# Performance work log

Measured on AMD Instinct MI355X. Metric: run time of the kernel, lower is better.

Reference implementation:

```python
import jax, jax.numpy as jnp
import numpy as np

N, E, F = 20000, 160000, 128
H, C1, C2 = 4, 128, 256
G, NCLS = 64, 10


def setup_inputs() -> dict:
    key = jax.random.key(0)
    ks = jax.random.split(key, 14)
    s = 0.05
    inp = {
        "x": jax.random.normal(ks[0], (N, F), jnp.float32),
        "edge_index": jax.random.randint(ks[1], (2, E), 0, N, dtype=jnp.int32),
        "batch": ((jnp.arange(N, dtype=jnp.int32) * G) // N),  # sorted graph ids, all 64 graphs non-empty
        # GATConv 1: in=128 -> 128 per head, heads=4, concat -> 512
        "W1": jax.random.normal(ks[2], (F, H * C1), jnp.float32) * s,
        "att_src1": jax.random.normal(ks[3], (H, C1), jnp.float32) * s,
        "att_dst1": jax.random.normal(ks[4], (H, C1), jnp.float32) * s,
        "b1": jnp.zeros((H * C1,), jnp.float32),
        # GATConv 2: in=512 -> 256, heads=1, concat=False
        "W2": jax.random.normal(ks[5], (H * C1, C2), jnp.float32) * s,
        "att_src2": jax.random.normal(ks[6], (1, C2), jnp.float32) * s,
        "att_dst2": jax.random.normal(ks[7], (1, C2), jnp.float32) * s,
        "b2": jnp.zeros((C2,), jnp.float32),
        # fc head
        "fc1_w": jax.random.normal(ks[8], (C2, 64), jnp.float32) * s,
        "fc1_b": jnp.zeros((64,), jnp.float32),
        "fc2_w": jax.random.normal(ks[9], (64, NCLS), jnp.float32) * s,
        "fc2_b": jnp.zeros((NCLS,), jnp.float32),
    }
    return inp


def gat_conv(x, src, dst, W, att_src, att_dst, bias, concat):
    """PyG GATConv: per-edge attention + segment softmax over dst + scatter-add."""
    n = x.shape[0]
    h_, c_ = att_src.shape
    h = (x @ W).reshape(n, h_, c_)                    # [N,H,C]
    a_src = jnp.einsum('nhc,hc->nh', h, att_src)       # [N,H]
    a_dst = jnp.einsum('nhc,hc->nh', h, att_dst)       # [N,H]
    e = jax.nn.leaky_relu(a_src[src] + a_dst[dst], negative_slope=0.2)  # [Etot,H]
    e_max = jax.ops.segment_max(e, dst, num_segments=n)
    ee = jnp.exp(e - e_max[dst])
    denom = jax.ops.segment_sum(ee, dst, num_segments=n)
    alpha = ee / denom[dst]                            # [Etot,H]
    out = jax.ops.segment_sum(h[src] * alpha[:, :, None], dst, num_segments=n)  # [N,H,C]
    out = out.reshape(n, h_ * c_) if concat else out.mean(axis=1)
    return out + bias


def reference(x, edge_index, batch, W1, att_src1, att_dst1, b1,
              W2, att_src2, att_dst2, b2, fc1_w, fc1_b, fc2_w, fc2_b):
    n = x.shape[0]
    # to_undirected: both directions; plus self-loops (GATConv add_self_loops=True)
    loops = jnp.arange(n, dtype=edge_index.dtype)
    src = jnp.concatenate([edge_index[0], edge_index[1], loops])
    dst = jnp.concatenate([edge_index[1], edge_index[0], loops])
    h = gat_conv(x, src, dst, W1, att_src1, att_dst1, b1, concat=True)
    h = jax.nn.relu(h)
    h = gat_conv(h, src, dst, W2, att_src2, att_dst2, b2, concat=False)
    g = jax.ops.segment_max(h, batch, num_segments=G)  # global_max_pool
    g = jax.nn.relu(g @ fc1_w + fc1_b) @ fc2_w + fc2_b
    return jax.nn.log_softmax(g, axis=1)
```

## Files before the change

### kernel.cpp

```cpp
#include <hip/hip_runtime.h>
#include <math.h>

#define FDIM 128
#define HEADS 4
#define C1DIM 128
#define C2DIM 256
#define NGRAPH 64
#define NCLS 10
#define DEGCAP 64

typedef __attribute__((ext_vector_type(8))) short short8;
typedef __attribute__((ext_vector_type(4))) float float4v;
typedef __attribute__((ext_vector_type(2))) float floatx2;

__device__ __forceinline__ unsigned short f2bf(float f) {
    unsigned u = __builtin_bit_cast(unsigned, f);
    unsigned r = (u + 0x7FFFu + ((u >> 16) & 1u)) >> 16;
    return (unsigned short)r;
}
__device__ __forceinline__ float bfu(unsigned short u) { return __builtin_bit_cast(float, (unsigned)u << 16); }
__device__ __forceinline__ float lrelu(float x) { return x > 0.f ? x : 0.2f * x; }
__device__ __forceinline__ float sel4(float a, float b, float c, float d, int hd) {
    return hd == 0 ? a : hd == 1 ? b : hd == 2 ? c : d;
}
__device__ __forceinline__ unsigned char f2fp8(float f) {
    return (unsigned char)(__builtin_amdgcn_cvt_pk_fp8_f32(f, f, 0, false) & 0xff);
}
__device__ __forceinline__ void fp8x8_dec(int2 r, float* f) {
    floatx2 p0 = __builtin_amdgcn_cvt_pk_f32_fp8(r.x, false);
    floatx2 p1 = __builtin_amdgcn_cvt_pk_f32_fp8(r.x, true);
    floatx2 p2 = __builtin_amdgcn_cvt_pk_f32_fp8(r.y, false);
    floatx2 p3 = __builtin_amdgcn_cvt_pk_f32_fp8(r.y, true);
    f[0] = p0.x; f[1] = p0.y; f[2] = p1.x; f[3] = p1.y;
    f[4] = p2.x; f[5] = p2.y; f[6] = p3.x; f[7] = p3.y;
}
__device__ __forceinline__ void fp8x4_dec(int r, float* f) {
    floatx2 p0 = __builtin_amdgcn_cvt_pk_f32_fp8(r, false);
    floatx2 p1 = __builtin_amdgcn_cvt_pk_f32_fp8(r, true);
    f[0] = p0.x; f[1] = p0.y; f[2] = p1.x; f[3] = p1.y;
}
__device__ __forceinline__ unsigned encf(float v) {
    unsigned b = __builtin_bit_cast(unsigned, v);
    return (b & 0x80000000u) ? ~b : (b | 0x80000000u);
}
__device__ __forceinline__ float decf(unsigned u) {
    unsigned b = (u & 0x80000000u) ? (u ^ 0x80000000u) : ~u;
    return __builtin_bit_cast(float, b);
}

__global__ __launch_bounds__(256) void prep_kernel(
        int* __restrict__ zero_base, int nzero_words,
        const float* __restrict__ x, unsigned short* __restrict__ xb, int n4,
        const float* __restrict__ W1, unsigned short* __restrict__ W1t,
        const float* __restrict__ W2, unsigned short* __restrict__ W2t,
        int ZB, int CB) {
    __shared__ float tile[32][33];
    int blk = blockIdx.x;
    if (blk < ZB) {
        int i = blk * 256 + threadIdx.x;
        if (i < nzero_words) zero_base[i] = 0;
        return;
    }
    blk -= ZB;
    if (blk < CB) {
        int i = blk * 256 + threadIdx.x;
        if (i < n4) {
            float4 v = ((const float4*)x)[i];
            ushort4 o;
            o.x = f2bf(v.x); o.y = f2bf(v.y); o.z = f2bf(v.z); o.w = f2bf(v.w);
            ((ushort4*)xb)[i] = o;
        }
        return;
    }
    blk -= CB;
    const float* W; unsigned short* Wt; int K, Nc, bx, by;
    if (blk < 64) {
        W = W1; Wt = W1t; K = 128; Nc = 512;
        bx = (blk & 15) * 32; by = (blk >> 4) * 32;
    } else {
        blk -= 64;
        W = W2; Wt = W2t; K = 512; Nc = 256;
        bx = (blk & 7) * 32; by = (blk >> 3) * 32;
    }
    int tx = threadIdx.x & 31, ty = threadIdx.x >> 5;
    #pragma unroll
    for (int r = 0; r < 32; r += 8)
        tile[ty + r][tx] = W[(size_t)(by + ty + r) * Nc + bx + tx];
    __syncthreads();
    #pragma unroll
    for (int r = 0; r < 32; r += 8)
        Wt[(size_t)(bx + ty + r) * K + by + tx] = f2bf(tile[tx][ty + r]);
}

template<int MODE>
__global__ __launch_bounds__(256) void bgemm_kernel(
        const unsigned short* __restrict__ A,
        const unsigned short* __restrict__ Bt,
        unsigned char* __restrict__ Cout,
        const float* __restrict__ att_src,
        const float* __restrict__ att_dst,
        float* __restrict__ as_out,
        float* __restrict__ ad_out,
        int M, int N_, int K,
        const int* __restrict__ ei, int E,
        int* __restrict__ cnt, int* __restrict__ esrc, int SB) {
    if (MODE == 1 && blockIdx.x < SB) {
        int i = blockIdx.x * 256 + threadIdx.x;
        if (i < 2 * E) {
            int src = ei[i];
            int dst = (i < E) ? ei[E + i] : ei[i - E];
            int pos = atomicAdd(&cnt[dst], 1);
            if (pos < DEGCAP) esrc[(dst << 6) + pos] = src;
        }
        return;
    }
    constexpr int BN = (MODE == 1) ? 128 : 256;
    constexpr int JW = BN / 32;
    constexpr int CPADB = BN + 16;
    constexpr int SMEMB = 4096 + BN * 64;
    __shared__ __align__(16) unsigned char smem[SMEMB];
    unsigned short* As = (unsigned short*)smem;
    unsigned short* Bs = (unsigned short*)(smem + 4096);
    __shared__ float sd_s[4][32];
    __shared__ float sd_d[4][32];
    const int t = threadIdx.x;
    const int lane = t & 63;
    const int wave = t >> 6;
    int row0, col0, headi;
    if (MODE == 1) {
        int bb = blockIdx.x - SB;
        headi = bb & 3;
        col0 = headi * BN;
        row0 = (bb >> 2) * 64;
    } else {
        headi = 0;
        col0 = 0;
        row0 = blockIdx.x * 64;
    }
    const int wr = (wave >> 1) * 32, wc = (wave & 1) * (BN / 2);
    float4v acc[2][JW] = {};
    for (int k0 = 0; k0 < K; k0 += 32) {
        {
            int i = t;
            int gr = row0 + (i >> 2); if (gr >= M) gr = M - 1;
            const unsigned short* gp = A + (size_t)gr * K + k0 + ((i & 3) << 3);
            __builtin_amdgcn_global_load_lds(
                (const __attribute__((address_space(1))) unsigned int*)gp,
                (__attribute__((address_space(3))) unsigned int*)&As[i * 8], 16, 0, 0);
        }
        #pragma unroll
        for (int c = 0; c < BN / 64; ++c) {
            int i = c * 256 + t;
            int gn = col0 + (i >> 2);
            const unsigned short* gp = Bt + (size_t)gn * K + k0 + ((i & 3) << 3);
            __builtin_amdgcn_global_load_lds(
                (const __attribute__((address_space(1))) unsigned int*)gp,
                (__attribute__((address_space(3))) unsigned int*)&Bs[i * 8], 16, 0, 0);
        }
        __syncthreads();
        short8 af[2], bfr[JW];
        #pragma unroll
        for (int i = 0; i < 2; ++i)
            af[i] = *(const short8*)&As[(wr + i * 16 + (lane & 15)) * 32 + (lane >> 4) * 8];
        #pragma unroll
        for (int j = 0; j < JW; ++j)
            bfr[j] = *(const short8*)&Bs[(wc + j * 16 + (lane & 15)) * 32 + (lane >> 4) * 8];
        #pragma unroll
        for (int i = 0; i < 2; ++i)
            #pragma unroll
            for (int j = 0; j < JW; ++j)
                acc[i][j] = __builtin_amdgcn_mfma_f32_16x16x32_bf16(af[i], bfr[j], acc[i][j], 0, 0, 0);
        __syncthreads();
    }
    float asv[JW], adv[JW];
    #pragma unroll
    for (int j = 0; j < JW; ++j) {
        int cc = col0 + wc + j * 16 + (lane & 15);
        asv[j] = att_src[cc];
        adv[j] = att_dst[cc];
    }
    #pragma unroll
    for (int i = 0; i < 2; ++i) {
        #pragma unroll
        for (int p = 0; p < 4; ++p) {
            int rr = wr + i * 16 + (lane >> 4) * 4 + p;
            float s = 0.f, d = 0.f;
            #pragma unroll
            for (int j = 0; j < JW; ++j) {
                smem[rr * CPADB + wc + j * 16 + (lane & 15)] = f2fp8(acc[i][j][p]);
                s += acc[i][j][p] * asv[j];
                d += acc[i][j][p] * adv[j];
            }
            #pragma unroll
            for (int o = 1; o <= 8; o <<= 1) { s += __shfl_xor(s, o); d += __shfl_xor(d, o); }
            if ((lane & 15) == 0) {
                int ridx = i * 16 + (lane >> 4) * 4 + p;
                sd_s[wave][ridx] = s;
                sd_d[wave][ridx] = d;
            }
        }
    }
    __syncthreads();
    #pragma unroll
    for (int it = 0; it < BN / 64; ++it) {
        int idx = it * 256 + t;
        int row = idx / (BN / 16), c16 = (idx % (BN / 16)) * 16;
        int grw = row0 + row;
        if (grw < M)
            *(int4*)&Cout[(size_t)grw * N_ + col0 + c16] = *(const int4*)&smem[row * CPADB + c16];
    }
    if ((wave & 1) == 0 && lane < 32) {
        float s = sd_s[wave][lane] + sd_s[wave + 1][lane];
        float d = sd_d[wave][lane] + sd_d[wave + 1][lane];
        int r = row0 + wr + lane;
        if (r < M) {
            if (MODE == 1) {
                as_out[r * 4 + headi] = s;
                ad_out[r * 4 + headi] = d;
            } else {
                as_out[r] = s;
                ad_out[r] = d;
            }
        }
    }
}

__global__ __launch_bounds__(256) void edge_agg1_kernel(
        const unsigned char* __restrict__ h1f8,
        const float4* __restrict__ as14,
        const float4* __restrict__ ad14,
        const int* __restrict__ cnt,
        const int* __restrict__ esrc,
        const float* __restrict__ b1,
        unsigned short* __restrict__ ho1b, int N) {
    __shared__ int sl_s[4][64];
    __shared__ __align__(16) float4 w_s[4][64];
    int wave = threadIdx.x >> 6, lane = threadIdx.x & 63;
    int node = blockIdx.x * 4 + wave;
    if (node >= N) return;
    int deg = cnt[node]; if (deg > DEGCAP) deg = DEGCAP;
    int ebase = node << 6;
    float4 asn = as14[node], adn = ad14[node];
    float w0 = __expf(lrelu(asn.x + adn.x));
    float w1 = __expf(lrelu(asn.y + adn.y));
    float w2 = __expf(lrelu(asn.z + adn.z));
    float w3 = __expf(lrelu(asn.w + adn.w));
    int hd = lane >> 4;
    int c0 = lane * 8;
    float wsh = sel4(w0, w1, w2, w3, hd);
    float acc[8];
    {
        int2 rs = *(const int2*)&h1f8[(size_t)node * 512 + c0];
        float f[8]; fp8x8_dec(rs, f);
        #pragma unroll
        for (int k = 0; k < 8; ++k) acc[k] = wsh * f[k];
    }
    float d0 = 0.f, d1 = 0.f, d2 = 0.f, d3 = 0.f;
    for (int cb = 0; cb < deg; cb += 64) {
        int idx = cb + lane;
        int sl = esrc[ebase + (idx < deg ? idx : deg - 1)];
        float4 wl = make_float4(0.f, 0.f, 0.f, 0.f);
        if (idx < deg) {
            float4 a = as14[sl];
            wl.x = __expf(lrelu(a.x + adn.x));
            wl.y = __expf(lrelu(a.y + adn.y));
            wl.z = __expf(lrelu(a.z + adn.z));
            wl.w = __expf(lrelu(a.w + adn.w));
            d0 += wl.x; d1 += wl.y; d2 += wl.z; d3 += wl.w;
        }
        sl_s[wave][lane] = sl;
        w_s[wave][lane] = wl;
        int jmax = deg - cb; if (jmax > 64) jmax = 64;
        int j = 0;
        for (; j + 4 <= jmax; j += 4) {
            int s0 = sl_s[wave][j],     s1 = sl_s[wave][j + 1];
            int s2 = sl_s[wave][j + 2], s3 = sl_s[wave][j + 3];
            float u0 = ((const float*)&w_s[wave][j])[hd];
            float u1 = ((const float*)&w_s[wave][j + 1])[hd];
            float u2 = ((const float*)&w_s[wave][j + 2])[hd];
            float u3 = ((const float*)&w_s[wave][j + 3])[hd];
            int2 r0 = *(const int2*)&h1f8[(size_t)s0 * 512 + c0];
            int2 r1 = *(const int2*)&h1f8[(size_t)s1 * 512 + c0];
            int2 r2 = *(const int2*)&h1f8[(size_t)s2 * 512 + c0];
            int2 r3 = *(const int2*)&h1f8[(size_t)s3 * 512 + c0];
            float f0[8], f1[8], f2[8], f3[8];
            fp8x8_dec(r0, f0); fp8x8_dec(r1, f1); fp8x8_dec(r2, f2); fp8x8_dec(r3, f3);
            #pragma unroll
            for (int k = 0; k < 8; ++k)
                acc[k] += u0 * f0[k] + u1 * f1[k] + u2 * f2[k] + u3 * f3[k];
        }
        for (; j < jmax; ++j) {
            int s = sl_s[wave][j];
            float u = ((const float*)&w_s[wave][j])[hd];
            int2 r = *(const int2*)&h1f8[(size_t)s * 512 + c0];
            float f[8]; fp8x8_dec(r, f);
            #pragma unroll
            for (int k = 0; k < 8; ++k) acc[k] += u * f[k];
        }
    }
    #pragma unroll
    for (int o = 32; o > 0; o >>= 1) {
        d0 += __shfl_xor(d0, o); d1 += __shfl_xor(d1, o);
        d2 += __shfl_xor(d2, o); d3 += __shfl_xor(d3, o);
    }
    d0 += w0; d1 += w1; d2 += w2; d3 += w3;
    float dh = sel4(d0, d1, d2, d3, hd);
    float inv = 1.f / dh;
    float4 bA = *(const float4*)&b1[c0], bB = *(const float4*)&b1[c0 + 4];
    float v0 = fmaxf(acc[0] * inv + bA.x, 0.f), v1 = fmaxf(acc[1] * inv + bA.y, 0.f);
    float v2 = fmaxf(acc[2] * inv + bA.z, 0.f), v3 = fmaxf(acc[3] * inv + bA.w, 0.f);
    float v4 = fmaxf(acc[4] * inv + bB.x, 0.f), v5 = fmaxf(acc[5] * inv + bB.y, 0.f);
    float v6 = fmaxf(acc[6] * inv + bB.z, 0.f), v7 = fmaxf(acc[7] * inv + bB.w, 0.f);
    int4 o;
    o.x = (int)((unsigned)f2bf(v0) | ((unsigned)f2bf(v1) << 16));
    o.y = (int)((unsigned)f2bf(v2) | ((unsigned)f2bf(v3) << 16));
    o.z = (int)((unsigned)f2bf(v4) | ((unsigned)f2bf(v5) << 16));
    o.w = (int)((unsigned)f2bf(v6) | ((unsigned)f2bf(v7) << 16));
    *(int4*)&ho1b[(size_t)node * 512 + c0] = o;
}

__global__ __launch_bounds__(256) void edge_agg2_kernel(
        const unsigned char* __restrict__ h2f8,
        const float* __restrict__ as2,
        const float* __restrict__ ad2,
        const int* __restrict__ cnt,
        const int* __restrict__ esrc,
        const float* __restrict__ b2,
        const int* __restrict__ batch,
        unsigned* __restrict__ pool, int N) {
    __shared__ unsigned pms[4][256];
    __shared__ int sl_s[4][64];
    __shared__ float w_s[4][64];
    int wave = threadIdx.x >> 6, lane = threadIdx.x & 63;
    int node = blockIdx.x * 4 + wave;
    bool valid = node < N;
    int c0 = lane * 4;
    unsigned e0 = 0, e1 = 0, e2 = 0, e3 = 0;
    if (valid) {
        int deg = cnt[node]; if (deg > DEGCAP) deg = DEGCAP;
        int ebase = node << 6;
        float adn = ad2[node];
        float wself = __expf(lrelu(as2[node] + adn));
        float a0, a1, a2, a3;
        {
            int r = *(const int*)&h2f8[(size_t)node * 256 + c0];
            float f[4]; fp8x4_dec(r, f);
            a0 = wself * f[0]; a1 = wself * f[1]; a2 = wself * f[2]; a3 = wself * f[3];
        }
        float dsum = 0.f;
        for (int cb = 0; cb < deg; cb += 64) {
            int idx = cb + lane;
            int sl = esrc[ebase + (idx < deg ? idx : deg - 1)];
            float wl = 0.f;
            if (idx < deg) {
                wl = __expf(lrelu(as2[sl] + adn));
                dsum += wl;
            }
            sl_s[wave][lane] = sl;
            w_s[wave][lane] = wl;
            int jmax = deg - cb; if (jmax > 64) jmax = 64;
            int j = 0;
            for (; j + 8 <= jmax; j += 8) {
                int ss[8]; float u[8]; int r[8];
                #pragma unroll
                for (int q = 0; q < 8; ++q) {
                    ss[q] = sl_s[wave][j + q];
                    u[q] = w_s[wave][j + q];
                }
                #pragma unroll
                for (int q = 0; q < 8; ++q) r[q] = *(const int*)&h2f8[(size_t)ss[q] * 256 + c0];
                #pragma unroll
                for (int q = 0; q < 8; ++q) {
                    float f[4]; fp8x4_dec(r[q], f);
                    a0 += u[q] * f[0]; a1 += u[q] * f[1];
                    a2 += u[q] * f[2]; a3 += u[q] * f[3];
                }
            }
            for (; j < jmax; ++j) {
                int s = sl_s[wave][j];
                float u = w_s[wave][j];
                int r = *(const int*)&h2f8[(size_t)s * 256 + c0];
                float f[4]; fp8x4_dec(r, f);
                a0 += u * f[0]; a1 += u * f[1]; a2 += u * f[2]; a3 += u * f[3];
            }
        }
        #pragma unroll
        for (int o = 32; o > 0; o >>= 1) dsum += __shfl_xor(dsum, o);
        dsum += wself;
        float inv = 1.f / dsum;
        float4 bv = *(const float4*)&b2[c0];
        e0 = encf(a0 * inv + bv.x);
        e1 = encf(a1 * inv + bv.y);
        e2 = encf(a2 * inv + bv.z);
        e3 = encf(a3 * inv + bv.w);
    }
    pms[wave][c0]     = e0;
    pms[wave][c0 + 1] = e1;
    pms[wave][c0 + 2] = e2;
    pms[wave][c0 + 3] = e3;
    __syncthreads();
    int n0 = blockIdx.x * 4;
    int n3 = n0 + 3; if (n3 >= N) n3 = N - 1;
    int g0 = batch[n0], g3 = batch[n3];
    if (g0 == g3) {
        int tt = threadIdx.x;
        unsigned m0 = pms[0][tt] > pms[1][tt] ? pms[0][tt] : pms[1][tt];
        unsigned m1 = pms[2][tt] > pms[3][tt] ? pms[2][tt] : pms[3][tt];
        unsigned m = m0 > m1 ? m0 : m1;
        atomicMax(&pool[(size_t)g0 * 256 + tt], m);
    } else if (valid) {
        int g = batch[node];
        atomicMax(&pool[(size_t)g * 256 + c0], e0);
        atomicMax(&pool[(size_t)g * 256 + c0 + 1], e1);
        atomicMax(&pool[(size_t)g * 256 + c0 + 2], e2);
        atomicMax(&pool[(size_t)g * 256 + c0 + 3], e3);
    }
}

__global__ __launch_bounds__(64) void head_kernel(const unsigned* __restrict__ pool,
                                                  const float* __restrict__ fc1w,
                                                  const float* __restrict__ fc1b,
                                                  const float* __restrict__ fc2w,
                                                  const float* __restrict__ fc2b,
                                                  float* __restrict__ out) {
    __shared__ float gr[256];
    __shared__ float hid[64];
    __shared__ float o10[NCLS];
    int g = blockIdx.x, t = threadIdx.x;
    for (int i = t; i < 256; i += 64)
        gr[i] = decf(pool[(size_t)g * 256 + i]);
    __syncthreads();
    float s = fc1b[t];
    for (int k = 0; k < 256; ++k) s += gr[k] * fc1w[k * 64 + t];
    hid[t] = s > 0.f ? s : 0.f;
    __syncthreads();
    if (t < NCLS) {
        float s2 = fc2b[t];
        for (int k = 0; k < 64; ++k) s2 += hid[k] * fc2w[k * NCLS + t];
        o10[t] = s2;
    }
    __syncthreads();
    if (t == 0) {
        float mx = -INFINITY;
        for (int c = 0; c < NCLS; ++c) mx = fmaxf(mx, o10[c]);
        float se = 0.f;
        for (int c = 0; c < NCLS; ++c) se += __expf(o10[c] - mx);
        float lse = mx + logf(se);
        for (int c = 0; c < NCLS; ++c) out[g * NCLS + c] = o10[c] - lse;
    }
}

extern "C" void kernel_launch(void* const* d_in, const int* in_sizes, int n_in,
                              void* d_out, int out_size, void* d_ws, size_t ws_size,
                              hipStream_t stream) {
    (void)n_in; (void)out_size; (void)ws_size;
    const float* x        = (const float*)d_in[0];
    const int*   ei       = (const int*)d_in[1];
    const int*   batch    = (const int*)d_in[2];
    const float* W1       = (const float*)d_in[3];
    const float* att_src1 = (const float*)d_in[4];
    const float* att_dst1 = (const float*)d_in[5];
    const float* b1       = (const float*)d_in[6];
    const float* W2       = (const float*)d_in[7];
    const float* att_src2 = (const float*)d_in[8];
    const float* att_dst2 = (const float*)d_in[9];
    const float* b2       = (const float*)d_in[10];
    const float* fc1w     = (const float*)d_in[11];
    const float* fc1b     = (const float*)d_in[12];
    const float* fc2w     = (const float*)d_in[13];
    const float* fc2b     = (const float*)d_in[14];

    const int N = in_sizes[2];
    const int E = in_sizes[1] / 2;
    const int tot = 2 * E;

    char* base = (char*)d_ws;
    size_t off = 0;
    auto alloc = [&](size_t bytes) -> void* {
        void* p = base + off;
        off = (off + bytes + 255) & ~(size_t)255;
        return p;
    };
    int*      cnt    = (int*)alloc((size_t)N * 4);
    unsigned* pool   = (unsigned*)alloc((size_t)NGRAPH * 256 * 4);
    size_t zend = off;
    int*   esrc   = (int*)alloc((size_t)N * DEGCAP * 4);
    float* as1    = (float*)alloc((size_t)N * HEADS * 4);
    float* ad1    = (float*)alloc((size_t)N * HEADS * 4);
    float* as2    = (float*)alloc((size_t)N * 4);
    float* ad2    = (float*)alloc((size_t)N * 4);
    unsigned short* xb   = (unsigned short*)alloc((size_t)N * FDIM * 2);
    unsigned short* W1t  = (unsigned short*)alloc((size_t)512 * 128 * 2);
    unsigned short* W2t  = (unsigned short*)alloc((size_t)256 * 512 * 2);
    unsigned char*  h1f8 = (unsigned char*)alloc((size_t)N * 512);
    unsigned short* ho1b = (unsigned short*)alloc((size_t)N * 512 * 2);
    unsigned char*  h2f8 = (unsigned char*)alloc((size_t)N * 256);

    int nzero = (int)((zend - (size_t)((char*)cnt - base)) / 4);
    int ZB = (nzero + 255) / 256;
    int n4 = N * FDIM / 4;
    int CB = (n4 + 255) / 256;
    prep_kernel<<<ZB + CB + 64 + 128, 256, 0, stream>>>(
        cnt, nzero, x, xb, n4, W1, W1t, W2, W2t, ZB, CB);

    int SB = (tot + 255) / 256;
    int rowb = (N + 63) / 64;
    bgemm_kernel<1><<<SB + 4 * rowb, 256, 0, stream>>>(
        xb, W1t, h1f8, att_src1, att_dst1, as1, ad1, N, 512, 128, ei, E, cnt, esrc, SB);

    edge_agg1_kernel<<<(N + 3) / 4, 256, 0, stream>>>(h1f8, (const float4*)as1, (const float4*)ad1,
                                                      cnt, esrc, b1, ho1b, N);

    bgemm_kernel<2><<<rowb, 256, 0, stream>>>(
        ho1b, W2t, h2f8, att_src2, att_dst2, as2, ad2, N, 256, 512,
        nullptr, 0, nullptr, nullptr, 0);

    edge_agg2_kernel<<<(N + 3) / 4, 256, 0, stream>>>(h2f8, as2, ad2, cnt, esrc, b2,
                                                      batch, pool, N);

    head_kernel<<<NGRAPH, 64, 0, stream>>>(pool, fc1w, fc1b, fc2w, fc2b, (float*)d_out);
}
```

Baseline: 189.2 us.

## Split edge aggregation across channel slices and parallelize edges within each wave

Both edge aggregation kernels now launch eight blocks per group of four nodes. Each block handles one channel slice: 64 channels, one head-half, for layer 1 and 32 channels for layer 2. Within a wave, lanes are split into edge sub-groups that process several edges at once and then combine partial sums with cross-lane shuffles, replacing the staging of source indices and weights in shared memory. This gives far more parallelism and many more loads in flight for the low-degree gathers. In exchange, each block recomputes the attention weights and reloads the edge indices, and there are more pooling atomics.

```diff
diff --git a/kernel.cpp b/kernel.cpp
--- a/kernel.cpp
+++ b/kernel.cpp
@@ -18,21 +18,9 @@
     unsigned r = (u + 0x7FFFu + ((u >> 16) & 1u)) >> 16;
     return (unsigned short)r;
 }
-__device__ __forceinline__ float bfu(unsigned short u) { return __builtin_bit_cast(float, (unsigned)u << 16); }
 __device__ __forceinline__ float lrelu(float x) { return x > 0.f ? x : 0.2f * x; }
-__device__ __forceinline__ float sel4(float a, float b, float c, float d, int hd) {
-    return hd == 0 ? a : hd == 1 ? b : hd == 2 ? c : d;
-}
 __device__ __forceinline__ unsigned char f2fp8(float f) {
     return (unsigned char)(__builtin_amdgcn_cvt_pk_fp8_f32(f, f, 0, false) & 0xff);
-}
-__device__ __forceinline__ void fp8x8_dec(int2 r, float* f) {
-    floatx2 p0 = __builtin_amdgcn_cvt_pk_f32_fp8(r.x, false);
-    floatx2 p1 = __builtin_amdgcn_cvt_pk_f32_fp8(r.x, true);
-    floatx2 p2 = __builtin_amdgcn_cvt_pk_f32_fp8(r.y, false);
-    floatx2 p3 = __builtin_amdgcn_cvt_pk_f32_fp8(r.y, true);
-    f[0] = p0.x; f[1] = p0.y; f[2] = p1.x; f[3] = p1.y;
-    f[4] = p2.x; f[5] = p2.y; f[6] = p3.x; f[7] = p3.y;
 }
 __device__ __forceinline__ void fp8x4_dec(int r, float* f) {
     floatx2 p0 = __builtin_amdgcn_cvt_pk_f32_fp8(r, false);
@@ -227,96 +215,59 @@
 
 __global__ __launch_bounds__(256) void edge_agg1_kernel(
         const unsigned char* __restrict__ h1f8,
-        const float4* __restrict__ as14,
-        const float4* __restrict__ ad14,
+        const float* __restrict__ as1,
+        const float* __restrict__ ad1,
         const int* __restrict__ cnt,
         const int* __restrict__ esrc,
         const float* __restrict__ b1,
         unsigned short* __restrict__ ho1b, int N) {
-    __shared__ int sl_s[4][64];
-    __shared__ __align__(16) float4 w_s[4][64];
+    int s = blockIdx.x & 7;
     int wave = threadIdx.x >> 6, lane = threadIdx.x & 63;
-    int node = blockIdx.x * 4 + wave;
+    int node = (blockIdx.x >> 3) * 4 + wave;
     if (node >= N) return;
+    int h = s >> 1;
+    int cb = s * 64;
+    int cw = lane & 15;
+    int es = lane >> 4;
     int deg = cnt[node]; if (deg > DEGCAP) deg = DEGCAP;
     int ebase = node << 6;
-    float4 asn = as14[node], adn = ad14[node];
-    float w0 = __expf(lrelu(asn.x + adn.x));
-    float w1 = __expf(lrelu(asn.y + adn.y));
-    float w2 = __expf(lrelu(asn.z + adn.z));
-    float w3 = __expf(lrelu(asn.w + adn.w));
-    int hd = lane >> 4;
-    int c0 = lane * 8;
-    float wsh = sel4(w0, w1, w2, w3, hd);
-    float acc[8];
+    float adn = ad1[node * 4 + h];
+    float wself = __expf(lrelu(as1[node * 4 + h] + adn));
+    float a0 = 0.f, a1 = 0.f, a2 = 0.f, a3 = 0.f;
     {
-        int2 rs = *(const int2*)&h1f8[(size_t)node * 512 + c0];
-        float f[8]; fp8x8_dec(rs, f);
-        #pragma unroll
-        for (int k = 0; k < 8; ++k) acc[k] = wsh * f[k];
-    }
-    float d0 = 0.f, d1 = 0.f, d2 = 0.f, d3 = 0.f;
-    for (int cb = 0; cb < deg; cb += 64) {
-        int idx = cb + lane;
-        int sl = esrc[ebase + (idx < deg ? idx : deg - 1)];
-        float4 wl = make_float4(0.f, 0.f, 0.f, 0.f);
-        if (idx < deg) {
-            float4 a = as14[sl];
-            wl.x = __expf(lrelu(a.x + adn.x));
-            wl.y = __expf(lrelu(a.y + adn.y));
-            wl.z = __expf(lrelu(a.z + adn.z));
-            wl.w = __expf(lrelu(a.w + adn.w));
-            d0 += wl.x; d1 += wl.y; d2 += wl.z; d3 += wl.w;
-        }
-        sl_s[wave][lane] = sl;
-        w_s[wave][lane] = wl;
-        int jmax = deg - cb; if (jmax > 64) jmax = 64;
-        int j = 0;
-        for (; j + 4 <= jmax; j += 4) {
-            int s0 = sl_s[wave][j],     s1 = sl_s[wave][j + 1];
-            int s2 = sl_s[wave][j + 2], s3 = sl_s[wave][j + 3];
-            float u0 = ((const float*)&w_s[wave][j])[hd];
-            float u1 = ((const float*)&w_s[wave][j + 1])[hd];
-            float u2 = ((const float*)&w_s[wave][j + 2])[hd];
-            float u3 = ((const float*)&w_s[wave][j + 3])[hd];
-            int2 r0 = *(const int2*)&h1f8[(size_t)s0 * 512 + c0];
-            int2 r1 = *(const int2*)&h1f8[(size_t)s1 * 512 + c0];
-            int2 r2 = *(const int2*)&h1f8[(size_t)s2 * 512 + c0];
-            int2 r3 = *(const int2*)&h1f8[(size_t)s3 * 512 + c0];
-            float f0[8], f1[8], f2[8], f3[8];
-            fp8x8_dec(r0, f0); fp8x8_dec(r1, f1); fp8x8_dec(r2, f2); fp8x8_dec(r3, f3);
-            #pragma unroll
-            for (int k = 0; k < 8; ++k)
-                acc[k] += u0 * f0[k] + u1 * f1[k] + u2 * f2[k] + u3 * f3[k];
-        }
-        for (; j < jmax; ++j) {
-            int s = sl_s[wave][j];
-            float u = ((const float*)&w_s[wave][j])[hd];
-            int2 r = *(const int2*)&h1f8[(size_t)s * 512 + c0];
-            float f[8]; fp8x8_dec(r, f);
-            #pragma unroll
-            for (int k = 0; k < 8; ++k) acc[k] += u * f[k];
-        }
-    }
-    #pragma unroll
-    for (int o = 32; o > 0; o >>= 1) {
-        d0 += __shfl_xor(d0, o); d1 += __shfl_xor(d1, o);
-        d2 += __shfl_xor(d2, o); d3 += __shfl_xor(d3, o);
-    }
-    d0 += w0; d1 += w1; d2 += w2; d3 += w3;
-    float dh = sel4(d0, d1, d2, d3, hd);
-    float inv = 1.f / dh;
-    float4 bA = *(const float4*)&b1[c0], bB = *(const float4*)&b1[c0 + 4];
-    float v0 = fmaxf(acc[0] * inv + bA.x, 0.f), v1 = fmaxf(acc[1] * inv + bA.y, 0.f);
-    float v2 = fmaxf(acc[2] * inv + bA.z, 0.f), v3 = fmaxf(acc[3] * inv + bA.w, 0.f);
-    float v4 = fmaxf(acc[4] * inv + bB.x, 0.f), v5 = fmaxf(acc[5] * inv + bB.y, 0.f);
-    float v6 = fmaxf(acc[6] * inv + bB.z, 0.f), v7 = fmaxf(acc[7] * inv + bB.w, 0.f);
-    int4 o;
-    o.x = (int)((unsigned)f2bf(v0) | ((unsigned)f2bf(v1) << 16));
-    o.y = (int)((unsigned)f2bf(v2) | ((unsigned)f2bf(v3) << 16));
-    o.z = (int)((unsigned)f2bf(v4) | ((unsigned)f2bf(v5) << 16));
-    o.w = (int)((unsigned)f2bf(v6) | ((unsigned)f2bf(v7) << 16));
-    *(int4*)&ho1b[(size_t)node * 512 + c0] = o;
+        int r = *(const int*)&h1f8[(size_t)node * 512 + cb + cw * 4];
+        float f[4]; fp8x4_dec(r, f);
+        if (es == 0) { a0 = wself * f[0]; a1 = wself * f[1]; a2 = wself * f[2]; a3 = wself * f[3]; }
+    }
+    float dsum = 0.f;
+    #pragma unroll 2
+    for (int e0 = 0; e0 < deg; e0 += 4) {
+        int e = e0 + es;
+        int src = esrc[ebase + (e < deg ? e : deg - 1)];
+        float w = 0.f;
+        if (e < deg) w = __expf(lrelu(as1[src * 4 + h] + adn));
+        if (cw == 0) dsum += w;
+        int r = *(const int*)&h1f8[(size_t)src * 512 + cb + cw * 4];
+        float f[4]; fp8x4_dec(r, f);
+        a0 += w * f[0]; a1 += w * f[1]; a2 += w * f[2]; a3 += w * f[3];
+    }
+    a0 += __shfl_xor(a0, 16); a0 += __shfl_xor(a0, 32);
+    a1 += __shfl_xor(a1, 16); a1 += __shfl_xor(a1, 32);
+    a2 += __shfl_xor(a2, 16); a2 += __shfl_xor(a2, 32);
+    a3 += __shfl_xor(a3, 16); a3 += __shfl_xor(a3, 32);
+    #pragma unroll
+    for (int o = 1; o <= 32; o <<= 1) dsum += __shfl_xor(dsum, o);
+    dsum += wself;
+    float inv = 1.f / dsum;
+    if (es == 0) {
+        float4 bv = *(const float4*)&b1[cb + cw * 4];
+        float v0 = fmaxf(a0 * inv + bv.x, 0.f), v1 = fmaxf(a1 * inv + bv.y, 0.f);
+        float v2 = fmaxf(a2 * inv + bv.z, 0.f), v3 = fmaxf(a3 * inv + bv.w, 0.f);
+        int2 o;
+        o.x = (int)((unsigned)f2bf(v0) | ((unsigned)f2bf(v1) << 16));
+        o.y = (int)((unsigned)f2bf(v2) | ((unsigned)f2bf(v3) << 16));
+        *(int2*)&ho1b[(size_t)node * 512 + cb + cw * 4] = o;
+    }
 }
 
 __global__ __launch_bounds__(256) void edge_agg2_kernel(
@@ -328,92 +279,76 @@
         const float* __restrict__ b2,
         const int* __restrict__ batch,
         unsigned* __restrict__ pool, int N) {
-    __shared__ unsigned pms[4][256];
-    __shared__ int sl_s[4][64];
-    __shared__ float w_s[4][64];
+    __shared__ unsigned pms[4][32];
+    int s = blockIdx.x & 7;
     int wave = threadIdx.x >> 6, lane = threadIdx.x & 63;
-    int node = blockIdx.x * 4 + wave;
+    int node = (blockIdx.x >> 3) * 4 + wave;
     bool valid = node < N;
-    int c0 = lane * 4;
-    unsigned e0 = 0, e1 = 0, e2 = 0, e3 = 0;
+    int cb = s * 32;
+    int cw = lane & 7;
+    int es = lane >> 3;
+    unsigned u0 = 0, u1 = 0, u2 = 0, u3 = 0;
     if (valid) {
         int deg = cnt[node]; if (deg > DEGCAP) deg = DEGCAP;
         int ebase = node << 6;
         float adn = ad2[node];
         float wself = __expf(lrelu(as2[node] + adn));
-        float a0, a1, a2, a3;
+        float a0 = 0.f, a1 = 0.f, a2 = 0.f, a3 = 0.f;
         {
-            int r = *(const int*)&h2f8[(size_t)node * 256 + c0];
+            int r = *(const int*)&h2f8[(size_t)node * 256 + cb + cw * 4];
             float f[4]; fp8x4_dec(r, f);
-            a0 = wself * f[0]; a1 = wself * f[1]; a2 = wself * f[2]; a3 = wself * f[3];
+            if (es == 0) { a0 = wself * f[0]; a1 = wself * f[1]; a2 = wself * f[2]; a3 = wself * f[3]; }
         }
         float dsum = 0.f;
-        for (int cb = 0; cb < deg; cb += 64) {
-            int idx = cb + lane;
-            int sl = esrc[ebase + (idx < deg ? idx : deg - 1)];
-            float wl = 0.f;
-            if (idx < deg) {
-                wl = __expf(lrelu(as2[sl] + adn));
-                dsum += wl;
-            }
-            sl_s[wave][lane] = sl;
-            w_s[wave][lane] = wl;
-            int jmax = deg - cb; if (jmax > 64) jmax = 64;
-            int j = 0;
-            for (; j + 8 <= jmax; j += 8) {
-                int ss[8]; float u[8]; int r[8];
-                #pragma unroll
-                for (int q = 0; q < 8; ++q) {
-                    ss[q] = sl_s[wave][j + q];
-                    u[q] = w_s[wave][j + q];
-                }
-                #pragma unroll
-                for (int q = 0; q < 8; ++q) r[q] = *(const int*)&h2f8[(size_t)ss[q] * 256 + c0];
-                #pragma unroll
-                for (int q = 0; q < 8; ++q) {
-                    float f[4]; fp8x4_dec(r[q], f);
-                    a0 += u[q] * f[0]; a1 += u[q] * f[1];
-                    a2 += u[q] * f[2]; a3 += u[q] * f[3];
-                }
-            }
-            for (; j < jmax; ++j) {
-                int s = sl_s[wave][j];
-                float u = w_s[wave][j];
-                int r = *(const int*)&h2f8[(size_t)s * 256 + c0];
-                float f[4]; fp8x4_dec(r, f);
-                a0 += u * f[0]; a1 += u * f[1]; a2 += u * f[2]; a3 += u * f[3];
-            }
-        }
-        #pragma unroll
-        for (int o = 32; o > 0; o >>= 1) dsum += __shfl_xor(dsum, o);
+        #pragma unroll 2
+        for (int e0 = 0; e0 < deg; e0 += 8) {
+            int e = e0 + es;
+            int src = esrc[ebase + (e < deg ? e : deg - 1)];
+            float w = 0.f;
+            if (e < deg) w = __expf(lrelu(as2[src] + adn));
+            if (cw == 0) dsum += w;
+            int r = *(const int*)&h2f8[(size_t)src * 256 + cb + cw * 4];
+            float f[4]; fp8x4_dec(r, f);
+            a0 += w * f[0]; a1 += w * f[1]; a2 += w * f[2]; a3 += w * f[3];
+        }
+        a0 += __shfl_xor(a0, 8); a0 += __shfl_xor(a0, 16); a0 += __shfl_xor(a0, 32);
+        a1 += __shfl_xor(a1, 8); a1 += __shfl_xor(a1, 16); a1 += __shfl_xor(a1, 32);
+        a2 += __shfl_xor(a2, 8); a2 += __shfl_xor(a2, 16); a2 += __shfl_xor(a2, 32);
+        a3 += __shfl_xor(a3, 8); a3 += __shfl_xor(a3, 16); a3 += __shfl_xor(a3, 32);
+        #pragma unroll
+        for (int o = 1; o <= 32; o <<= 1) dsum += __shfl_xor(dsum, o);
         dsum += wself;
         float inv = 1.f / dsum;
-        float4 bv = *(const float4*)&b2[c0];
-        e0 = encf(a0 * inv + bv.x);
-        e1 = encf(a1 * inv + bv.y);
-        e2 = encf(a2 * inv + bv.z);
-        e3 = encf(a3 * inv + bv.w);
-    }
-    pms[wave][c0]     = e0;
-    pms[wave][c0 + 1] = e1;
-    pms[wave][c0 + 2] = e2;
-    pms[wave][c0 + 3] = e3;
-    __syncthreads();
-    int n0 = blockIdx.x * 4;
+        float4 bv = *(const float4*)&b2[cb + cw * 4];
+        u0 = encf(a0 * inv + bv.x);
+        u1 = encf(a1 * inv + bv.y);
+        u2 = encf(a2 * inv + bv.z);
+        u3 = encf(a3 * inv + bv.w);
+    }
+    if (es == 0) {
+        pms[wave][cw * 4]     = u0;
+        pms[wave][cw * 4 + 1] = u1;
+        pms[wave][cw * 4 + 2] = u2;
+        pms[wave][cw * 4 + 3] = u3;
+    }
+    __syncthreads();
+    int n0 = (blockIdx.x >> 3) * 4;
     int n3 = n0 + 3; if (n3 >= N) n3 = N - 1;
     int g0 = batch[n0], g3 = batch[n3];
     if (g0 == g3) {
         int tt = threadIdx.x;
-        unsigned m0 = pms[0][tt] > pms[1][tt] ? pms[0][tt] : pms[1][tt];
-        unsigned m1 = pms[2][tt] > pms[3][tt] ? pms[2][tt] : pms[3][tt];
-        unsigned m = m0 > m1 ? m0 : m1;
-        atomicMax(&pool[(size_t)g0 * 256 + tt], m);
-    } else if (valid) {
+        if (tt < 32) {
+            unsigned m0 = pms[0][tt] > pms[1][tt] ? pms[0][tt] : pms[1][tt];
+            unsigned m1 = pms[2][tt] > pms[3][tt] ? pms[2][tt] : pms[3][tt];
+            unsigned m = m0 > m1 ? m0 : m1;
+            atomicMax(&pool[(size_t)g0 * 256 + cb + tt], m);
+        }
+    } else if (valid && es == 0) {
         int g = batch[node];
-        atomicMax(&pool[(size_t)g * 256 + c0], e0);
-        atomicMax(&pool[(size_t)g * 256 + c0 + 1], e1);
-        atomicMax(&pool[(size_t)g * 256 + c0 + 2], e2);
-        atomicMax(&pool[(size_t)g * 256 + c0 + 3], e3);
+        atomicMax(&pool[(size_t)g * 256 + cb + cw * 4],     u0);
+        atomicMax(&pool[(size_t)g * 256 + cb + cw * 4 + 1], u1);
+        atomicMax(&pool[(size_t)g * 256 + cb + cw * 4 + 2], u2);
+        atomicMax(&pool[(size_t)g * 256 + cb + cw * 4 + 3], u3);
     }
 }
 
@@ -508,15 +443,15 @@
     bgemm_kernel<1><<<SB + 4 * rowb, 256, 0, stream>>>(
         xb, W1t, h1f8, att_src1, att_dst1, as1, ad1, N, 512, 128, ei, E, cnt, esrc, SB);
 
-    edge_agg1_kernel<<<(N + 3) / 4, 256, 0, stream>>>(h1f8, (const float4*)as1, (const float4*)ad1,
-                                                      cnt, esrc, b1, ho1b, N);
+    edge_agg1_kernel<<<((N + 3) / 4) * 8, 256, 0, stream>>>(h1f8, as1, ad1,
+                                                            cnt, esrc, b1, ho1b, N);
 
     bgemm_kernel<2><<<rowb, 256, 0, stream>>>(
         ho1b, W2t, h2f8, att_src2, att_dst2, as2, ad2, N, 256, 512,
         nullptr, 0, nullptr, nullptr, 0);
 
-    edge_agg2_kernel<<<(N + 3) / 4, 256, 0, stream>>>(h2f8, as2, ad2, cnt, esrc, b2,
-                                                      batch, pool, N);
+    edge_agg2_kernel<<<((N + 3) / 4) * 8, 256, 0, stream>>>(h2f8, as2, ad2, cnt, esrc, b2,
+                                                            batch, pool, N);
 
     head_kernel<<<NGRAPH, 64, 0, stream>>>(pool, fc1w, fc1b, fc2w, fc2b, (float*)d_out);
 }
```

After: 306.1 us. 1.62x slower.
